# Performance work log

Hardware: AMD Instinct MI355X
Metric: run time of the kernel (lower is better)

Reference implementation:

```python
import jax, jax.numpy as jnp
import numpy as np

PAD = 0
SIGMA_C = 2.0
EPS = 1e-6
LOG_SQRT_2PI = 0.9189385332046727  # log(sqrt(2*pi))

B, T_CHAR, VOCAB, D_EMB = 32, 256, 100, 384


def setup_inputs() -> dict:
    rng = np.random.default_rng(0)
    # text tokens in [1, VOCAB): avoid pad (=0) inside the utterance
    text = rng.integers(1, VOCAB, size=(B, T_CHAR), dtype=np.int64)
    # per-char durations in frames, 1..8
    durs = rng.integers(1, 9, size=(B, T_CHAR), dtype=np.int32)
    # total_time = length of repeat_interleave(text, durs) padded to batch max
    total_time = int(durs.sum(axis=-1).max())
    key = jax.random.key(0)
    embed = jax.random.normal(key, (VOCAB, D_EMB), dtype=jnp.float32)
    return {
        "text": jnp.asarray(text),
        "durs": jnp.asarray(durs),
        "embed": embed,
        "total_time": total_time,
    }


def reference(text, durs, embed, total_time):
    # Pad 2 trailing positions: pad token, zero duration (as in the original)
    text = jnp.pad(text, ((0, 0), (0, 2)), constant_values=PAD)      # [B, Tc]
    durs = jnp.pad(durs, ((0, 0), (0, 2)), constant_values=0)        # [B, Tc]
    durs_f = durs.astype(jnp.float32)

    # Gaussian centers: mid-point of each char's frame span
    csum = jnp.cumsum(durs_f, axis=-1)
    c = durs_f / 2.0 + jnp.pad(csum[:, :-1], ((0, 0), (1, 0)))       # [B, Tc]
    sig = durs_f / SIGMA_C + EPS                                     # [B, Tc]

    t = jnp.arange(total_time, dtype=jnp.float32) + 0.5              # [Tt]

    # Gaussian pdf evaluated at frame times: w[b, t, c]
    z = (t[None, :, None] - c[:, None, :]) / sig[:, None, :]         # [B, Tt, Tc]
    w = jnp.exp(-0.5 * z * z - jnp.log(sig)[:, None, :] - LOG_SQRT_2PI)

    # zero padded-char columns, normalize over chars
    char_pad = (text == PAD)[:, None, :]                             # [B, 1, Tc]
    w = jnp.where(char_pad, 0.0, w)
    w = w / (jnp.sum(w, axis=-1, keepdims=True) + EPS)

    # time positions past each utterance's total duration are padding:
    # zero the whole row, then put weight 1.0 on the last (pad) char column
    total_dur = jnp.sum(durs, axis=-1)                               # [B]
    time_pad = jnp.arange(total_time)[None, :] >= total_dur[:, None] # [B, Tt]
    w = jnp.where(time_pad[:, :, None], 0.0, w)
    w = w.at[:, :, -1].set(jnp.where(time_pad, 1.0, w[:, :, -1]))

    # aggregate gathered embeddings: [B, Tt, Tc] x [B, Tc, D] -> [B, Tt, D]
    u = jnp.einsum("btc,bcd->btd", w, embed[text])
    return u
```

## Files before the change

kernel.cpp:

```cpp
#include <hip/hip_runtime.h>

#define TC 256
#define DEMB 384
#define VOC 100
#define WIN 96
#define TTILE 32
#define WPS 104
#define LOG_SQRT_2PI 0.9189385332046727f

typedef short v8s __attribute__((ext_vector_type(8)));
typedef float v4f __attribute__((ext_vector_type(4)));

__device__ __forceinline__ unsigned short f32_to_bf16_rne(float f) {
    union { float f; unsigned int u; } x; x.f = f;
    unsigned int u = x.u;
    return (unsigned short)((u + 0x7FFFu + ((u >> 16) & 1u)) >> 16);
}

__global__ __launch_bounds__(256) void embed_transpose_kernel(
    const float* __restrict__ embed, unsigned short* __restrict__ embT)
{
    int i = blockIdx.x * 256 + threadIdx.x;
    if (i >= DEMB * VOC) return;
    int n = i / VOC, v = i - n * VOC;
    embT[i] = f32_to_bf16_rne(embed[v * DEMB + n]);
}

__global__ __launch_bounds__(256) void gauss_embed_mfma_kernel(
    const int* __restrict__ text,
    const int* __restrict__ durs,
    const float* __restrict__ embed,
    const unsigned short* __restrict__ embT,
    float* __restrict__ out,
    int Tt)
{
    const int b   = blockIdx.y;
    const int t0  = blockIdx.x * TTILE;
    const int tid = threadIdx.x;
    const int wv   = tid >> 6;
    const int lane = tid & 63;
    const int nq   = lane & 15;
    const int q    = lane >> 4;

    __shared__ __align__(16) unsigned short s_embT[DEMB * VOC];
    __shared__ __align__(16) unsigned short s_wp[TTILE * WPS];
    __shared__ float s_scan[TC];
    __shared__ float s_part[256];
    __shared__ float s_invS[TTILE];
    __shared__ int   s_wtx[WIN];
    __shared__ int   s_j0, s_totdur;

    s_scan[tid] = (float)durs[b * TC + tid];
    if (tid == 0) s_j0 = TC - 1;
    __syncthreads();
    for (int ofs = 1; ofs < TC; ofs <<= 1) {
        float v = (tid >= ofs) ? s_scan[tid - ofs] : 0.0f;
        __syncthreads();
        s_scan[tid] += v;
        __syncthreads();
    }

    {
        int en = (int)s_scan[tid];
        int st = tid ? (int)s_scan[tid - 1] : 0;
        if (t0 >= st && t0 < en) s_j0 = tid;
        if (tid == 0) s_totdur = (int)s_scan[TC - 1];
    }
    __syncthreads();

    int base = s_j0 - 31;
    base = base < 0 ? 0 : (base > TC - WIN ? TC - WIN : base);
    const int totdur = s_totdur;

    {
        const char* gsrc = (const char*)embT;
        for (int ch = wv; ch < 75; ch += 4) {
            __builtin_amdgcn_global_load_lds(
                (const __attribute__((address_space(1))) unsigned int*)(gsrc + ch * 1024 + lane * 16),
                (__attribute__((address_space(3))) unsigned int*)((char*)s_embT + ch * 1024),
                16, 0, 0);
        }
    }

    {
        const int t = tid & 31;
        const int g = tid >> 5;
        const float tf = (float)(t0 + t) + 0.5f;
        float lsum = 0.0f;
#pragma unroll
        for (int cc = 0; cc < 12; ++cc) {
            int c = g * 12 + cc;
            int j = base + c;
            float endf   = s_scan[j];
            float startf = j ? s_scan[j - 1] : 0.0f;
            float dur = endf - startf;
            float sig = dur * 0.5f + 1e-6f;
            float ctr = endf - dur * 0.5f;
            float z = (tf - ctr) / sig;
            float w = __expf(fmaf(-0.5f * z, z, -__logf(sig) - LOG_SQRT_2PI));
            lsum += w;
            s_wp[t * WPS + c] = f32_to_bf16_rne(w);
        }
        s_part[tid] = lsum;
        if (tid < WIN) s_wtx[tid] = text[b * TC + base + tid];
    }
    __syncthreads();

    if (tid < TTILE) {
        float s = 1e-6f;
#pragma unroll
        for (int g = 0; g < 8; ++g) s += s_part[g * 32 + tid];
        s_invS[tid] = 1.0f / s;
    }
    __syncthreads();

    v4f acc[6][2];
#pragma unroll
    for (int nt = 0; nt < 6; ++nt)
#pragma unroll
        for (int mt = 0; mt < 2; ++mt) {
            v4f z = {0.0f, 0.0f, 0.0f, 0.0f};
            acc[nt][mt] = z;
        }

#pragma unroll
    for (int ks = 0; ks < 3; ++ks) {
        const int c0 = ks * 32;
        int vidx[8];
#pragma unroll
        for (int j = 0; j < 8; ++j) vidx[j] = s_wtx[c0 + q * 8 + j];
        v8s a0 = *(const v8s*)(s_wp + nq * WPS + c0 + q * 8);
        v8s a1 = *(const v8s*)(s_wp + (16 + nq) * WPS + c0 + q * 8);
#pragma unroll
        for (int nt = 0; nt < 6; ++nt) {
            const unsigned short* col = s_embT + (wv * 96 + nt * 16 + nq) * VOC;
            v8s bf;
#pragma unroll
            for (int j = 0; j < 8; ++j) bf[j] = (short)col[vidx[j]];
            acc[nt][0] = __builtin_amdgcn_mfma_f32_16x16x32_bf16(a0, bf, acc[nt][0], 0, 0, 0);
            acc[nt][1] = __builtin_amdgcn_mfma_f32_16x16x32_bf16(a1, bf, acc[nt][1], 0, 0, 0);
        }
    }

    float pe[6];
#pragma unroll
    for (int nt = 0; nt < 6; ++nt) pe[nt] = embed[wv * 96 + nt * 16 + nq];

#pragma unroll
    for (int mt = 0; mt < 2; ++mt) {
#pragma unroll
        for (int r = 0; r < 4; ++r) {
            int tl = mt * 16 + q * 4 + r;
            int t = t0 + tl;
            if (t >= Tt) continue;
            float sv = s_invS[tl];
            bool pad = (t >= totdur);
            float* orow = out + (size_t)(b * Tt + t) * DEMB + wv * 96 + nq;
#pragma unroll
            for (int nt = 0; nt < 6; ++nt) {
                float val = pad ? pe[nt] : acc[nt][mt][r] * sv;
                orow[nt * 16] = val;
            }
        }
    }
}

extern "C" void kernel_launch(void* const* d_in, const int* in_sizes, int n_in,
                              void* d_out, int out_size, void* d_ws, size_t ws_size,
                              hipStream_t stream) {
    const int*   text  = (const int*)d_in[0];
    const int*   durs  = (const int*)d_in[1];
    const float* embed = (const float*)d_in[2];
    float* out = (float*)d_out;

    const int B = 32;
    const int Tt = out_size / (B * DEMB);

    unsigned short* embT = (unsigned short*)d_ws;
    embed_transpose_kernel<<<(DEMB * VOC + 255) / 256, 256, 0, stream>>>(embed, embT);

    dim3 grid((Tt + TTILE - 1) / TTILE, B);
    gauss_embed_mfma_kernel<<<grid, 256, 0, stream>>>(text, durs, embed, embT, out, Tt);
}
```

Measured before the change: 106.0 us.

## Pre-gather per-batch transposed bf16 embeddings and drop full-table LDS staging

A preprocessing kernel now gathers embed[text] for every batch and character into a transposed bf16 buffer laid out as [B, D, 288]. The main kernel no longer copies the whole 100x384 table into LDS or gathers scalar elements by token index; it loads contiguous 8-element B fragments straight from global memory. The window base is aligned to a multiple of 8 so those vector loads stay aligned. LDS use falls sharply, and launch bounds now ask for 4 blocks per CU. The cost is a larger preprocessing write of about 7 MB, written with strided 2-byte stores, plus global reads inside the MFMA loop.

Measured after the change: 101.2 us. 1.05x faster.

```diff
diff --git a/kernel.cpp b/kernel.cpp
--- a/kernel.cpp
+++ b/kernel.cpp
@@ -6,6 +6,7 @@
 #define WIN 96
 #define TTILE 32
 #define WPS 104
+#define CST 288
 #define LOG_SQRT_2PI 0.9189385332046727f
 
 typedef short v8s __attribute__((ext_vector_type(8)));
@@ -17,20 +18,34 @@
     return (unsigned short)((u + 0x7FFFu + ((u >> 16) & 1u)) >> 16);
 }
 
-__global__ __launch_bounds__(256) void embed_transpose_kernel(
-    const float* __restrict__ embed, unsigned short* __restrict__ embT)
+__global__ __launch_bounds__(256) void gather_transpose_kernel(
+    const int* __restrict__ text, const float* __restrict__ embed,
+    unsigned short* __restrict__ ET)
 {
     int i = blockIdx.x * 256 + threadIdx.x;
-    if (i >= DEMB * VOC) return;
-    int n = i / VOC, v = i - n * VOC;
-    embT[i] = f32_to_bf16_rne(embed[v * DEMB + n]);
+    int c = i % CST;
+    int r = i / CST;
+    int nseg = r & 3;
+    int b = r >> 2;
+    if (c >= TC || b >= 32) return;
+    int v = text[b * TC + c];
+    const float* erow = embed + (size_t)v * DEMB + nseg * 96;
+    unsigned short* dst = ET + ((size_t)b * DEMB + nseg * 96) * CST + c;
+#pragma unroll
+    for (int k = 0; k < 24; ++k) {
+        float4 e = *(const float4*)(erow + 4 * k);
+        dst[(4 * k + 0) * CST] = f32_to_bf16_rne(e.x);
+        dst[(4 * k + 1) * CST] = f32_to_bf16_rne(e.y);
+        dst[(4 * k + 2) * CST] = f32_to_bf16_rne(e.z);
+        dst[(4 * k + 3) * CST] = f32_to_bf16_rne(e.w);
+    }
 }
 
-__global__ __launch_bounds__(256) void gauss_embed_mfma_kernel(
+__global__ __launch_bounds__(256, 4) void gauss_embed_mfma_kernel(
     const int* __restrict__ text,
     const int* __restrict__ durs,
     const float* __restrict__ embed,
-    const unsigned short* __restrict__ embT,
+    const unsigned short* __restrict__ ET,
     float* __restrict__ out,
     int Tt)
 {
@@ -42,12 +57,10 @@
     const int nq   = lane & 15;
     const int q    = lane >> 4;
 
-    __shared__ __align__(16) unsigned short s_embT[DEMB * VOC];
-    __shared__ __align__(16) unsigned short s_wp[TTILE * WPS];
     __shared__ float s_scan[TC];
     __shared__ float s_part[256];
+    __shared__ __align__(16) unsigned short s_wp[TTILE * WPS];
     __shared__ float s_invS[TTILE];
-    __shared__ int   s_wtx[WIN];
     __shared__ int   s_j0, s_totdur;
 
     s_scan[tid] = (float)durs[b * TC + tid];
@@ -69,18 +82,10 @@
     __syncthreads();
 
     int base = s_j0 - 31;
-    base = base < 0 ? 0 : (base > TC - WIN ? TC - WIN : base);
+    base = base < 0 ? 0 : base;
+    base &= ~7;
+    base = base > TC - WIN ? TC - WIN : base;
     const int totdur = s_totdur;
-
-    {
-        const char* gsrc = (const char*)embT;
-        for (int ch = wv; ch < 75; ch += 4) {
-            __builtin_amdgcn_global_load_lds(
-                (const __attribute__((address_space(1))) unsigned int*)(gsrc + ch * 1024 + lane * 16),
-                (__attribute__((address_space(3))) unsigned int*)((char*)s_embT + ch * 1024),
-                16, 0, 0);
-        }
-    }
 
     {
         const int t = tid & 31;
@@ -102,7 +107,6 @@
             s_wp[t * WPS + c] = f32_to_bf16_rne(w);
         }
         s_part[tid] = lsum;
-        if (tid < WIN) s_wtx[tid] = text[b * TC + base + tid];
     }
     __syncthreads();
 
@@ -113,6 +117,8 @@
         s_invS[tid] = 1.0f / s;
     }
     __syncthreads();
+
+    const unsigned short* ETb = ET + (size_t)b * DEMB * CST;
 
     v4f acc[6][2];
 #pragma unroll
@@ -125,18 +131,12 @@
 
 #pragma unroll
     for (int ks = 0; ks < 3; ++ks) {
-        const int c0 = ks * 32;
-        int vidx[8];
-#pragma unroll
-        for (int j = 0; j < 8; ++j) vidx[j] = s_wtx[c0 + q * 8 + j];
-        v8s a0 = *(const v8s*)(s_wp + nq * WPS + c0 + q * 8);
-        v8s a1 = *(const v8s*)(s_wp + (16 + nq) * WPS + c0 + q * 8);
+        const int c0 = ks * 32 + q * 8;
+        v8s a0 = *(const v8s*)(s_wp + nq * WPS + c0);
+        v8s a1 = *(const v8s*)(s_wp + (16 + nq) * WPS + c0);
 #pragma unroll
         for (int nt = 0; nt < 6; ++nt) {
-            const unsigned short* col = s_embT + (wv * 96 + nt * 16 + nq) * VOC;
-            v8s bf;
-#pragma unroll
-            for (int j = 0; j < 8; ++j) bf[j] = (short)col[vidx[j]];
+            v8s bf = *(const v8s*)(ETb + (size_t)(wv * 96 + nt * 16 + nq) * CST + base + c0);
             acc[nt][0] = __builtin_amdgcn_mfma_f32_16x16x32_bf16(a0, bf, acc[nt][0], 0, 0, 0);
             acc[nt][1] = __builtin_amdgcn_mfma_f32_16x16x32_bf16(a1, bf, acc[nt][1], 0, 0, 0);
         }
@@ -176,9 +176,12 @@
     const int B = 32;
     const int Tt = out_size / (B * DEMB);
 
-    unsigned short* embT = (unsigned short*)d_ws;
-    embed_transpose_kernel<<<(DEMB * VOC + 255) / 256, 256, 0, stream>>>(embed, embT);
+    unsigned short* ET = (unsigned short*)d_ws;
+    {
+        int nthreads = 32 * 4 * CST;
+        gather_transpose_kernel<<<(nthreads + 255) / 256, 256, 0, stream>>>(text, embed, ET);
+    }
 
     dim3 grid((Tt + TTILE - 1) / TTILE, B);
-    gauss_embed_mfma_kernel<<<grid, 256, 0, stream>>>(text, durs, embed, embT, out, Tt);
+    gauss_embed_mfma_kernel<<<grid, 256, 0, stream>>>(text, durs, embed, ET, out, Tt);
 }
```
